# Kernel optimization log

Hardware: AMD Instinct MI355X
Metric: run time of the kernel (lower is better)

Reference implementation:

```python
import jax, jax.numpy as jnp
import numpy as np
from jax import lax

B, CIN, COUT, K, N = 128, 32, 64, 3, 56
TAU, BETA = 0.5, 4.0


def _build_templates(n, tau, beta):
    # dist[mu_i, mu_j, i, j] = |i-mu_i| + |j-mu_j|
    r = np.arange(n)
    dist = np.abs(r[:, None, None, None] - r[None, None, :, None]) + \
           np.abs(r[None, :, None, None] - r[None, None, None, :])
    tpos = tau * np.maximum(1.0 - beta * dist / n, -1.0)          # [n,n,n,n]
    tpos = tpos.reshape(n * n, n, n).astype(np.float32)
    tneg = np.full((1, n, n), -tau, dtype=np.float32)
    return np.concatenate([tpos, tneg], axis=0)                   # [n*n+1, n, n]


def setup_inputs() -> dict:
    key = jax.random.key(0)
    k1, k2, k3 = jax.random.split(key, 3)
    x = jax.random.normal(k1, (B, CIN, N, N), dtype=jnp.float32)
    W = jax.random.normal(k2, (COUT, CIN, K, K), dtype=jnp.float32) * 0.05
    b = jax.random.normal(k3, (COUT,), dtype=jnp.float32) * 0.05
    templates = jnp.asarray(_build_templates(N, TAU, BETA))
    return {"x": x, "W": W, "b": b, "templates": templates}


def reference(x, W, b, templates):
    # conv2d padding=1, stride 1 + ReLU
    y = lax.conv_general_dilated(
        x, W, window_strides=(1, 1), padding=[(1, 1), (1, 1)],
        dimension_numbers=("NCHW", "OIHW", "NCHW"))
    y = jax.nn.relu(y + b[None, :, None, None])                   # [B,C,H,W]
    Bc, C, H, Wd = y.shape
    # per-(batch,channel) argmax over flattened spatial map -> template index
    idx = jnp.argmax(y.reshape(Bc, C, H * Wd), axis=-1)           # [B,C] int
    masks = templates[idx]                                        # [B,C,H,W]
    masked = y * masks
    return masked * (masked > 0)
```

## Files before the change

kernel.cpp:

```cpp
#include <hip/hip_runtime.h>
#include <cstddef>

#define NSP   56
#define NPX   3136
#define CINN  32
#define COUTN 64
#define NB    128
#define CO_PB 8
#define NSTRIP 14
#define THR   256
#define XCOL  64

__global__ __launch_bounds__(THR)
void wtrans(const float* __restrict__ W, float* __restrict__ w2)
{
    int idx = blockIdx.x * THR + threadIdx.x;
    if (idx < COUTN * CINN * 9) {
        int co_l = idx & 7;
        int t    = idx >> 3;
        int c    = t & 31;
        t >>= 5;
        int kk   = t % 9;
        int cog  = t / 9;
        w2[idx] = W[(size_t)(cog * 8 + co_l) * (CINN * 9) + c * 9 + kk];
    }
}

__global__ __launch_bounds__(THR, 3)
void conv_emul_pass1(const float* __restrict__ x,
                     const float* __restrict__ w2,
                     const float* __restrict__ bias,
                     float* __restrict__ y,
                     int* __restrict__ amax)
{
    __shared__ float xs[CINN][6][XCOL];
    __shared__ float rv[4][CO_PB];
    __shared__ int   ri[4][CO_PB];

    const int tid = threadIdx.x;
    const int ty  = tid >> 6;
    const int tx  = tid & 63;
    const int b       = blockIdx.x >> 3;
    const int cog     = blockIdx.x & 7;
    const int co_base = cog * CO_PB;

    const float* xb = x  + (size_t)b * CINN * NPX;
    const float* wq = w2 + (size_t)cog * (9 * CINN * CO_PB);

    float v1[CO_PB]; int i1[CO_PB];
    #pragma unroll
    for (int co = 0; co < CO_PB; ++co) { v1[co] = -1.f; i1[co] = 0; }

    float* yo = y + (size_t)(b * COUTN + co_base) * NPX;

    #pragma unroll 1
    for (int g = 0; g < NSTRIP; ++g) {
        if (g) __syncthreads();

        #pragma unroll 1
        for (int q = tid; q < CINN * 6 * 14; q += THR) {
            int c   = q / 84;
            int rem = q - c * 84;
            int r6  = rem / 14;
            int v4  = rem - r6 * 14;
            int gr  = 4 * g + r6 - 1;
            float4 val = make_float4(0.f, 0.f, 0.f, 0.f);
            if ((unsigned)gr < (unsigned)NSP)
                val = *(const float4*)(xb + (size_t)c * NPX + gr * NSP + 4 * v4);
            *(float4*)&xs[c][r6][4 + 4 * v4] = val;
        }
        if (tid < CINN * 6) {
            int c = tid / 6, r6 = tid - 6 * (tid / 6);
            xs[c][r6][3]  = 0.f;
            xs[c][r6][60] = 0.f;
        }
        __syncthreads();

        float acc[CO_PB];
        #pragma unroll
        for (int co = 0; co < CO_PB; ++co) acc[co] = 0.f;

        if (tx < NSP) {
            #pragma unroll
            for (int kh = 0; kh < 3; ++kh) {
                #pragma unroll
                for (int kw = 0; kw < 3; ++kw) {
                    const float* wk = wq + (kh * 3 + kw) * (CINN * CO_PB);
                    #pragma unroll 4
                    for (int c = 0; c < CINN; ++c) {
                        float xv = xs[c][ty + kh][tx + kw + 3];
                        #pragma unroll
                        for (int co = 0; co < CO_PB; ++co)
                            acc[co] = fmaf(xv, wk[c * CO_PB + co], acc[co]);
                    }
                }
            }
            int p = (4 * g + ty) * NSP + tx;
            #pragma unroll
            for (int co = 0; co < CO_PB; ++co) {
                float v = acc[co] + bias[co_base + co];
                v = fmaxf(v, 0.f);
                yo[(size_t)co * NPX + p] = v;
                if (v > v1[co]) { v1[co] = v; i1[co] = p; }
            }
        }
    }

    #pragma unroll
    for (int co = 0; co < CO_PB; ++co) {
        float bv = v1[co]; int bi = i1[co];
        #pragma unroll
        for (int off = 32; off > 0; off >>= 1) {
            float ov = __shfl_xor(bv, off);
            int   oi = __shfl_xor(bi, off);
            if (ov > bv || (ov == bv && oi < bi)) { bv = ov; bi = oi; }
        }
        if ((tid & 63) == 0) { rv[ty][co] = bv; ri[ty][co] = bi; }
    }
    __syncthreads();
    if (tid < CO_PB) {
        float bv = rv[0][tid]; int bi = ri[0][tid];
        #pragma unroll
        for (int w = 1; w < 4; ++w) {
            float ov = rv[w][tid]; int oi = ri[w][tid];
            if (ov > bv || (ov == bv && oi < bi)) { bv = ov; bi = oi; }
        }
        amax[b * COUTN + co_base + tid] = bi;
    }
}

__global__ __launch_bounds__(THR)
void mask_apply_pass2(float* __restrict__ y,
                      const float* __restrict__ tmpl,
                      const int* __restrict__ amax)
{
    const int bc = blockIdx.x;
    const int idx = amax[bc];
    const float* tp = tmpl + (size_t)idx * NPX;
    float* yp = y + (size_t)bc * NPX;
    #pragma unroll 1
    for (int p = threadIdx.x; p < NPX; p += THR) {
        float v = yp[p] * tp[p];
        yp[p] = v > 0.f ? v : 0.f;
    }
}

extern "C" void kernel_launch(void* const* d_in, const int* in_sizes, int n_in,
                              void* d_out, int out_size, void* d_ws, size_t ws_size,
                              hipStream_t stream)
{
    (void)in_sizes; (void)n_in; (void)ws_size; (void)out_size;
    const float* x  = (const float*)d_in[0];
    const float* W  = (const float*)d_in[1];
    const float* bi = (const float*)d_in[2];
    const float* tm = (const float*)d_in[3];
    float* out = (float*)d_out;
    int*   amax = (int*)d_ws;
    float* w2   = (float*)((char*)d_ws + 32768);

    hipLaunchKernelGGL(wtrans, dim3(72), dim3(THR), 0, stream, W, w2);

    dim3 grid1(NB * (COUTN / CO_PB));
    hipLaunchKernelGGL(conv_emul_pass1, grid1, dim3(THR), 0, stream,
                       x, w2, bi, out, amax);

    dim3 grid2(NB * COUTN);
    hipLaunchKernelGGL(mask_apply_pass2, grid2, dim3(THR), 0, stream,
                       out, tm, amax);
}
```

Before: 403.8 us.

## Enlarge conv row strips to 7 rows with 448 threads and vectorize mask pass

The conv kernel now processes 7 output rows per strip with 448 threads (8 strips instead of 14), using a row-major shared tile whose halo columns are zeroed once and whose rows are each loaded by one float4 per thread. For each tap, the 32 input-channel values are hoisted into registers before the FMA loop. The aim is to cut strip iterations, barriers and load index math, and to amortize the halo rows over more output rows. The mask pass now uses float4 loads and stores. The 32-value register array and the larger block may raise register pressure and limit occupancy.

```diff
diff --git a/kernel.cpp b/kernel.cpp
--- a/kernel.cpp
+++ b/kernel.cpp
@@ -7,14 +7,16 @@
 #define COUTN 64
 #define NB    128
 #define CO_PB 8
-#define NSTRIP 14
-#define THR   256
-#define XCOL  64
+#define ROWS  7
+#define NSTRIP 8
+#define THR   448
+#define SROWS 9
+#define XCOL  68
 
-__global__ __launch_bounds__(THR)
+__global__ __launch_bounds__(256)
 void wtrans(const float* __restrict__ W, float* __restrict__ w2)
 {
-    int idx = blockIdx.x * THR + threadIdx.x;
+    int idx = blockIdx.x * 256 + threadIdx.x;
     if (idx < COUTN * CINN * 9) {
         int co_l = idx & 7;
         int t    = idx >> 3;
@@ -26,16 +28,16 @@
     }
 }
 
-__global__ __launch_bounds__(THR, 3)
+__global__ __launch_bounds__(THR, 4)
 void conv_emul_pass1(const float* __restrict__ x,
                      const float* __restrict__ w2,
                      const float* __restrict__ bias,
                      float* __restrict__ y,
                      int* __restrict__ amax)
 {
-    __shared__ float xs[CINN][6][XCOL];
-    __shared__ float rv[4][CO_PB];
-    __shared__ int   ri[4][CO_PB];
+    __shared__ float xs[SROWS][CINN][XCOL];
+    __shared__ float rv[7][CO_PB];
+    __shared__ int   ri[7][CO_PB];
 
     const int tid = threadIdx.x;
     const int ty  = tid >> 6;
@@ -47,6 +49,17 @@
     const float* xb = x  + (size_t)b * CINN * NPX;
     const float* wq = w2 + (size_t)cog * (9 * CINN * CO_PB);
 
+    const int sc = tid / 14;
+    const int sv = tid - sc * 14;
+    const float* xg = xb + (size_t)sc * NPX + 4 * sv;
+
+    for (int t = tid; t < SROWS * CINN * 2; t += THR) {
+        int rr  = t / (CINN * 2);
+        int rem = t - rr * (CINN * 2);
+        int c   = rem >> 1;
+        xs[rr][c][(rem & 1) ? 60 : 3] = 0.f;
+    }
+
     float v1[CO_PB]; int i1[CO_PB];
     #pragma unroll
     for (int co = 0; co < CO_PB; ++co) { v1[co] = -1.f; i1[co] = 0; }
@@ -57,22 +70,13 @@
     for (int g = 0; g < NSTRIP; ++g) {
         if (g) __syncthreads();
 
-        #pragma unroll 1
-        for (int q = tid; q < CINN * 6 * 14; q += THR) {
-            int c   = q / 84;
-            int rem = q - c * 84;
-            int r6  = rem / 14;
-            int v4  = rem - r6 * 14;
-            int gr  = 4 * g + r6 - 1;
+        #pragma unroll
+        for (int rr = 0; rr < SROWS; ++rr) {
+            int gr = 7 * g + rr - 1;
             float4 val = make_float4(0.f, 0.f, 0.f, 0.f);
             if ((unsigned)gr < (unsigned)NSP)
-                val = *(const float4*)(xb + (size_t)c * NPX + gr * NSP + 4 * v4);
-            *(float4*)&xs[c][r6][4 + 4 * v4] = val;
-        }
-        if (tid < CINN * 6) {
-            int c = tid / 6, r6 = tid - 6 * (tid / 6);
-            xs[c][r6][3]  = 0.f;
-            xs[c][r6][60] = 0.f;
+                val = *(const float4*)(xg + gr * NSP);
+            *(float4*)&xs[rr][sc][4 + 4 * sv] = val;
         }
         __syncthreads();
 
@@ -85,17 +89,20 @@
             for (int kh = 0; kh < 3; ++kh) {
                 #pragma unroll
                 for (int kw = 0; kw < 3; ++kw) {
+                    float xv[CINN];
+                    #pragma unroll
+                    for (int c = 0; c < CINN; ++c)
+                        xv[c] = xs[ty + kh][c][tx + kw + 3];
                     const float* wk = wq + (kh * 3 + kw) * (CINN * CO_PB);
-                    #pragma unroll 4
+                    #pragma unroll
                     for (int c = 0; c < CINN; ++c) {
-                        float xv = xs[c][ty + kh][tx + kw + 3];
                         #pragma unroll
                         for (int co = 0; co < CO_PB; ++co)
-                            acc[co] = fmaf(xv, wk[c * CO_PB + co], acc[co]);
+                            acc[co] = fmaf(xv[c], wk[c * CO_PB + co], acc[co]);
                     }
                 }
             }
-            int p = (4 * g + ty) * NSP + tx;
+            int p = (7 * g + ty) * NSP + tx;
             #pragma unroll
             for (int co = 0; co < CO_PB; ++co) {
                 float v = acc[co] + bias[co_base + co];
@@ -121,7 +128,7 @@
     if (tid < CO_PB) {
         float bv = rv[0][tid]; int bi = ri[0][tid];
         #pragma unroll
-        for (int w = 1; w < 4; ++w) {
+        for (int w = 1; w < 7; ++w) {
             float ov = rv[w][tid]; int oi = ri[w][tid];
             if (ov > bv || (ov == bv && oi < bi)) { bv = ov; bi = oi; }
         }
@@ -129,19 +136,25 @@
     }
 }
 
-__global__ __launch_bounds__(THR)
+__global__ __launch_bounds__(256)
 void mask_apply_pass2(float* __restrict__ y,
                       const float* __restrict__ tmpl,
                       const int* __restrict__ amax)
 {
     const int bc = blockIdx.x;
     const int idx = amax[bc];
-    const float* tp = tmpl + (size_t)idx * NPX;
-    float* yp = y + (size_t)bc * NPX;
+    const float4* tp = (const float4*)(tmpl + (size_t)idx * NPX);
+    float4* yp = (float4*)(y + (size_t)bc * NPX);
     #pragma unroll 1
-    for (int p = threadIdx.x; p < NPX; p += THR) {
-        float v = yp[p] * tp[p];
-        yp[p] = v > 0.f ? v : 0.f;
+    for (int p = threadIdx.x; p < NPX / 4; p += 256) {
+        float4 a = yp[p];
+        float4 t = tp[p];
+        a.x *= t.x; a.y *= t.y; a.z *= t.z; a.w *= t.w;
+        a.x = a.x > 0.f ? a.x : 0.f;
+        a.y = a.y > 0.f ? a.y : 0.f;
+        a.z = a.z > 0.f ? a.z : 0.f;
+        a.w = a.w > 0.f ? a.w : 0.f;
+        yp[p] = a;
     }
 }
 
@@ -158,13 +171,13 @@
     int*   amax = (int*)d_ws;
     float* w2   = (float*)((char*)d_ws + 32768);
 
-    hipLaunchKernelGGL(wtrans, dim3(72), dim3(THR), 0, stream, W, w2);
+    hipLaunchKernelGGL(wtrans, dim3(72), dim3(256), 0, stream, W, w2);
 
     dim3 grid1(NB * (COUTN / CO_PB));
     hipLaunchKernelGGL(conv_emul_pass1, grid1, dim3(THR), 0, stream,
                        x, w2, bi, out, amax);
 
     dim3 grid2(NB * COUTN);
-    hipLaunchKernelGGL(mask_apply_pass2, grid2, dim3(THR), 0, stream,
+    hipLaunchKernelGGL(mask_apply_pass2, grid2, dim3(256), 0, stream,
                        out, tm, amax);
 }
```

Measured after the change: 415.8 us. 3.0% more time.
